# Optimization experiments

Hardware: AMD Instinct MI355X
Metric: run time of the kernel (lower is better)

Reference implementation:

```python
import jax, jax.numpy as jnp
import numpy as np

L, H, NH, PF = 2, 256, 8, 512
D = H // NH
SCALE = float(np.sqrt(D))  # transformerCPI scales by sqrt(hid_dim // n_heads)


def layernorm(x, g, b, eps=1e-5):
    m = x.mean(-1, keepdims=True)
    v = ((x - m) ** 2).mean(-1, keepdims=True)
    return (x - m) / jnp.sqrt(v + eps) * g + b


def mha(q, k, v, wq, bq, wk, bk, wv, bv, wo, bo):
    B, Tq, _ = q.shape
    Tk = k.shape[1]
    Q = (q @ wq + bq).reshape(B, Tq, NH, D).transpose(0, 2, 1, 3)  # [B,h,Tq,d]
    K = (k @ wk + bk).reshape(B, Tk, NH, D).transpose(0, 2, 1, 3)
    V = (v @ wv + bv).reshape(B, Tk, NH, D).transpose(0, 2, 1, 3)
    att = jax.nn.softmax(jnp.einsum('bhqd,bhkd->bhqk', Q, K) / SCALE, axis=-1)
    x = jnp.einsum('bhqk,bhkd->bhqd', att, V).transpose(0, 2, 1, 3).reshape(B, Tq, H)
    return x @ wo + bo, att


def setup_inputs() -> dict:
    key = jax.random.key(0)
    ks = iter(jax.random.split(key, 64))
    B, T, S, A = 16, 512, 1024, 64
    p = lambda shape: jax.random.normal(next(ks), shape, jnp.float32) * 0.02
    inp = {
        'trg': jax.random.normal(next(ks), (B, T, A), jnp.float32),
        'src': jax.random.normal(next(ks), (B, S, H), jnp.float32),
        'ft_w': p((A, H)), 'ft_b': jnp.zeros((H,), jnp.float32),
        'fc1_w': p((H, 256)), 'fc1_b': jnp.zeros((256,), jnp.float32),
        'fc2_w': p((256, 2)), 'fc2_b': jnp.zeros((2,), jnp.float32),
        'ln_g': jnp.ones((L, H), jnp.float32), 'ln_b': jnp.zeros((L, H), jnp.float32),
        'pf_w1': p((L, H, PF)), 'pf_b1': jnp.zeros((L, PF), jnp.float32),
        'pf_w2': p((L, PF, H)), 'pf_b2': jnp.zeros((L, H), jnp.float32),
    }
    for pre in ('sa', 'ea'):
        for nm in ('q', 'k', 'v', 'o'):
            inp[f'{pre}_w{nm}'] = p((L, H, H))
            inp[f'{pre}_b{nm}'] = jnp.zeros((L, H), jnp.float32)
    return inp


def reference(trg, src, ft_w, ft_b, sa_wq, sa_bq, sa_wk, sa_bk, sa_wv, sa_bv, sa_wo, sa_bo,
              ea_wq, ea_bq, ea_wk, ea_bk, ea_wv, ea_bv, ea_wo, ea_bo,
              pf_w1, pf_b1, pf_w2, pf_b2, ln_g, ln_b, fc1_w, fc1_b, fc2_w, fc2_b):
    x = trg @ ft_w + ft_b  # [B,T,H]
    att = None
    for l in range(L):  # small fixed layer count
        sa_out, _ = mha(x, x, x, sa_wq[l], sa_bq[l], sa_wk[l], sa_bk[l],
                        sa_wv[l], sa_bv[l], sa_wo[l], sa_bo[l])
        x = layernorm(x + sa_out, ln_g[l], ln_b[l])
        ea_out, att = mha(x, src, src, ea_wq[l], ea_bq[l], ea_wk[l], ea_bk[l],
                          ea_wv[l], ea_bv[l], ea_wo[l], ea_bo[l])
        x = layernorm(x + ea_out, ln_g[l], ln_b[l])
        ff = jax.nn.relu(x @ pf_w1[l] + pf_b1[l]) @ pf_w2[l] + pf_b2[l]
        x = layernorm(x + ff, ln_g[l], ln_b[l])
    # norm-based softmax pooling (vectorized form of the original double loop)
    w = jax.nn.softmax(jnp.linalg.norm(x, axis=2), axis=1)  # [B,T]
    pooled = jnp.einsum('bt,bth->bh', w, x)                 # [B,H]
    label = jax.nn.relu(pooled @ fc1_w + fc1_b) @ fc2_w + fc2_b  # [B,2]
    return label, pooled, att
```

## Files before the change

### kernel.cpp

```cpp
#include <hip/hip_runtime.h>


typedef __bf16 bfrag __attribute__((ext_vector_type(8)));
typedef float f32x4 __attribute__((ext_vector_type(4)));
typedef unsigned int uint4v __attribute__((ext_vector_type(4)));

__device__ __forceinline__ unsigned short f2bf(float x) {
  unsigned u = __float_as_uint(x);
  u += 0x7fff + ((u >> 16) & 1);
  return (unsigned short)(u >> 16);
}
__device__ __forceinline__ float bf2f(unsigned short h) {
  return __uint_as_float((unsigned)h << 16);
}
__device__ __forceinline__ void split2(float x, unsigned short& hi, unsigned short& lo) {
  hi = f2bf(x);
  lo = f2bf(x - bf2f(hi));
}

__global__ __launch_bounds__(256) void wsplit(
    const float* __restrict__ W, short* __restrict__ Th, short* __restrict__ Tl,
    int K, int N)
{
  __shared__ float t[32][33];
  const int n0 = blockIdx.x * 32, k0 = blockIdx.y * 32;
  const int tx = threadIdx.x & 31, ty = threadIdx.x >> 5;
#pragma unroll
  for (int p = 0; p < 4; p++)
    t[ty + p * 8][tx] = W[(size_t)(k0 + ty + p * 8) * N + n0 + tx];
  __syncthreads();
#pragma unroll
  for (int p = 0; p < 4; p++) {
    float v = t[tx][ty + p * 8];
    unsigned short hi, lo; split2(v, hi, lo);
    size_t o = (size_t)(n0 + ty + p * 8) * K + k0 + tx;
    Th[o] = (short)hi; Tl[o] = (short)lo;
  }
}

__global__ __launch_bounds__(256) void xsplit(
    const float* __restrict__ X, short* __restrict__ Xh, short* __restrict__ Xl,
    int n4)
{
  int i = blockIdx.x * 256 + threadIdx.x;
  if (i < n4) {
    float4 v = ((const float4*)X)[i];
    ushort4 h, l;
    split2(v.x, h.x, l.x); split2(v.y, h.y, l.y);
    split2(v.z, h.z, l.z); split2(v.w, h.w, l.w);
    ((ushort4*)Xh)[i] = h; ((ushort4*)Xl)[i] = l;
  }
}

template <bool RELU, bool SPLIT, bool WRITE_C, bool VT>
__global__ __launch_bounds__(256) void gemm_mfma(
    const short* __restrict__ Ah_g, const short* __restrict__ Al_g,
    const short* __restrict__ Bh_g, const short* __restrict__ Bl_g,
    const float* __restrict__ bias, float* __restrict__ C,
    short* __restrict__ Ch, short* __restrict__ Cl,
    int M, int N, int K, int tksh)
{
  __shared__ short Ah[64 * 40], Al[64 * 40], Bh[64 * 40], Bl[64 * 40];
  const int tid = threadIdx.x;
  const int lane = tid & 63, w = tid >> 6;
  const int wm = w & 1, wn = w >> 1;
  const int m0 = blockIdx.x * 64, n0 = blockIdx.y * 64;
  const int srow = tid >> 2, sc4 = tid & 3;
  const int l15 = lane & 15, l4 = lane >> 4;
  f32x4 acc[2][2] = {};

  for (int k0 = 0; k0 < K; k0 += 32) {
    {
      const size_t ga = (size_t)(m0 + srow) * K + k0 + sc4 * 8;
      const size_t gb = (size_t)(n0 + srow) * K + k0 + sc4 * 8;
      uint4 va_h = *(const uint4*)(Ah_g + ga);
      uint4 va_l = *(const uint4*)(Al_g + ga);
      uint4 vb_h = *(const uint4*)(Bh_g + gb);
      uint4 vb_l = *(const uint4*)(Bl_g + gb);
      const int so = srow * 40 + sc4 * 8;
      *(uint4*)(Ah + so) = va_h;  *(uint4*)(Al + so) = va_l;
      *(uint4*)(Bh + so) = vb_h;  *(uint4*)(Bl + so) = vb_l;
    }
    __syncthreads();
    bfrag af_h[2], af_l[2], bf_h[2], bf_l[2];
#pragma unroll
    for (int mi = 0; mi < 2; mi++) {
      int r = wm * 32 + mi * 16 + l15;
      af_h[mi] = *(const bfrag*)(Ah + r * 40 + l4 * 8);
      af_l[mi] = *(const bfrag*)(Al + r * 40 + l4 * 8);
    }
#pragma unroll
    for (int ni = 0; ni < 2; ni++) {
      int r = wn * 32 + ni * 16 + l15;
      bf_h[ni] = *(const bfrag*)(Bh + r * 40 + l4 * 8);
      bf_l[ni] = *(const bfrag*)(Bl + r * 40 + l4 * 8);
    }
#pragma unroll
    for (int mi = 0; mi < 2; mi++)
#pragma unroll
      for (int ni = 0; ni < 2; ni++) {
        acc[mi][ni] = __builtin_amdgcn_mfma_f32_16x16x32_bf16(af_h[mi], bf_h[ni], acc[mi][ni], 0, 0, 0);
        acc[mi][ni] = __builtin_amdgcn_mfma_f32_16x16x32_bf16(af_h[mi], bf_l[ni], acc[mi][ni], 0, 0, 0);
        acc[mi][ni] = __builtin_amdgcn_mfma_f32_16x16x32_bf16(af_l[mi], bf_h[ni], acc[mi][ni], 0, 0, 0);
      }
    __syncthreads();
  }
#pragma unroll
  for (int mi = 0; mi < 2; mi++)
#pragma unroll
    for (int ni = 0; ni < 2; ni++) {
      const int n = n0 + wn * 32 + ni * 16 + l15;
      const float bv = bias[n];
      if constexpr (VT) {
        const int m = m0 + wm * 32 + mi * 16 + l4 * 4;
        const int bb = m >> tksh, tt = m & ((1 << tksh) - 1);
        const size_t o = ((((size_t)bb * 8 + (n >> 5)) * 32 + (n & 31)) << tksh) + tt;
        unsigned long long wh = 0, wl = 0;
#pragma unroll
        for (int r = 0; r < 4; r++) {
          float v = acc[mi][ni][r] + bv;
          unsigned short hh, ll; split2(v, hh, ll);
          wh |= (unsigned long long)hh << (16 * r);
          wl |= (unsigned long long)ll << (16 * r);
        }
        *(unsigned long long*)(Ch + o) = wh;
        *(unsigned long long*)(Cl + o) = wl;
      } else {
#pragma unroll
        for (int r = 0; r < 4; r++) {
          const int m = m0 + wm * 32 + mi * 16 + l4 * 4 + r;
          float v = acc[mi][ni][r] + bv;
          if (RELU) v = fmaxf(v, 0.f);
          const size_t o = (size_t)m * N + n;
          if constexpr (WRITE_C) C[o] = v;
          if constexpr (SPLIT) {
            unsigned short hh, ll; split2(v, hh, ll);
            Ch[o] = (short)hh; Cl[o] = (short)ll;
          }
        }
      }
    }
}

template <int TK>
__global__ __launch_bounds__(256) void attn_mfma(
    const short* __restrict__ Qh, const short* __restrict__ Ql,
    const short* __restrict__ Kh, const short* __restrict__ Kl,
    const short* __restrict__ Vth, const short* __restrict__ Vtl,
    short* __restrict__ Oh, short* __restrict__ Ol,
    float* __restrict__ att_out)
{
  __shared__ float sc[16 * TK];
  const int b = blockIdx.z, h = blockIdx.y, q0 = blockIdx.x * 16;
  const int tid = threadIdx.x;
  const int lane = tid & 63, w = tid >> 6;
  const int l15 = lane & 15, l4 = lane >> 4;
  const float inv_scale = 0.17677669529663687f;

  const size_t qbase = (((size_t)b * 512 + q0 + l15) * 8 + h) * 32 + l4 * 8;
  bfrag qh = *(const bfrag*)(Qh + qbase);
  bfrag ql = *(const bfrag*)(Ql + qbase);

#pragma unroll 4
  for (int t = 0; t < TK / 64; t++) {
    const int n0c = w * (TK / 4) + t * 16;
    const size_t kbase = (((size_t)b * TK + n0c + l15) * 8 + h) * 32 + l4 * 8;
    bfrag kh = *(const bfrag*)(Kh + kbase);
    bfrag kl = *(const bfrag*)(Kl + kbase);
    f32x4 acc = {};
    acc = __builtin_amdgcn_mfma_f32_16x16x32_bf16(qh, kh, acc, 0, 0, 0);
    acc = __builtin_amdgcn_mfma_f32_16x16x32_bf16(qh, kl, acc, 0, 0, 0);
    acc = __builtin_amdgcn_mfma_f32_16x16x32_bf16(ql, kh, acc, 0, 0, 0);
    const int col = n0c + l15;
#pragma unroll
    for (int r = 0; r < 4; r++) {
      const int row = l4 * 4 + r;
      sc[row * TK + ((((col >> 2) ^ (row & 7)) << 2) | (col & 3))] = acc[r] * inv_scale;
    }
  }
  __syncthreads();

  const int sr = tid >> 4, sj = tid & 15, srsw = sr & 7;
  float mx = -1e30f;
  for (int k = sj; k < TK; k += 16)
    mx = fmaxf(mx, sc[sr * TK + ((((k >> 2) ^ srsw) << 2) | (k & 3))]);
#pragma unroll
  for (int off = 8; off > 0; off >>= 1) mx = fmaxf(mx, __shfl_xor(mx, off, 16));
  float sum = 0.f;
  for (int k = sj; k < TK; k += 16) {
    const int idx = sr * TK + ((((k >> 2) ^ srsw) << 2) | (k & 3));
    float e = __expf(sc[idx] - mx);
    sc[idx] = e;
    sum += e;
  }
#pragma unroll
  for (int off = 8; off > 0; off >>= 1) sum += __shfl_xor(sum, off, 16);
  const float inv = 1.f / sum;
  __syncthreads();

  if (att_out) {
    const size_t orow = (((size_t)(b * 8 + h)) * 512 + q0 + sr) * TK;
    for (int t = 0; t < TK / 64; t++) {
      const int g = sj + 16 * t;
      float4 e4 = *(const float4*)&sc[sr * TK + ((g ^ srsw) << 2)];
      e4.x *= inv; e4.y *= inv; e4.z *= inv; e4.w *= inv;
      *(float4*)&att_out[orow + g * 4] = e4;
    }
  }

  f32x4 oa0 = {}, oa1 = {};
  const float* pr = sc + l15 * TK;
  const int psw = l15 & 7;
  const size_t vb0 = (((size_t)(b * 8 + h)) * 32 + l15) * TK;
  for (int kc = w * (TK / 4); kc < (w + 1) * (TK / 4); kc += 32) {
    const int g0 = (kc >> 2) + l4 * 2;
    float4 p0 = *(const float4*)(pr + ((g0 ^ psw) << 2));
    float4 p1 = *(const float4*)(pr + (((g0 + 1) ^ psw) << 2));
    float f[8] = {p0.x, p0.y, p0.z, p0.w, p1.x, p1.y, p1.z, p1.w};
    uint4v uh, ul;
#pragma unroll
    for (int i = 0; i < 4; i++) {
      unsigned short h0, l0, h1, l1;
      split2(f[2 * i], h0, l0); split2(f[2 * i + 1], h1, l1);
      uh[i] = (unsigned)h0 | ((unsigned)h1 << 16);
      ul[i] = (unsigned)l0 | ((unsigned)l1 << 16);
    }
    bfrag ph = __builtin_bit_cast(bfrag, uh);
    bfrag pl = __builtin_bit_cast(bfrag, ul);
    const size_t vk = vb0 + kc + l4 * 8;
    bfrag v0h = *(const bfrag*)(Vth + vk);
    bfrag v0l = *(const bfrag*)(Vtl + vk);
    bfrag v1h = *(const bfrag*)(Vth + vk + (size_t)16 * TK);
    bfrag v1l = *(const bfrag*)(Vtl + vk + (size_t)16 * TK);
    oa0 = __builtin_amdgcn_mfma_f32_16x16x32_bf16(ph, v0h, oa0, 0, 0, 0);
    oa0 = __builtin_amdgcn_mfma_f32_16x16x32_bf16(ph, v0l, oa0, 0, 0, 0);
    oa0 = __builtin_amdgcn_mfma_f32_16x16x32_bf16(pl, v0h, oa0, 0, 0, 0);
    oa1 = __builtin_amdgcn_mfma_f32_16x16x32_bf16(ph, v1h, oa1, 0, 0, 0);
    oa1 = __builtin_amdgcn_mfma_f32_16x16x32_bf16(ph, v1l, oa1, 0, 0, 0);
    oa1 = __builtin_amdgcn_mfma_f32_16x16x32_bf16(pl, v1h, oa1, 0, 0, 0);
  }
  __syncthreads();
  float* obuf = sc;
#pragma unroll
  for (int r = 0; r < 4; r++) {
    obuf[(w * 16 + l4 * 4 + r) * 32 + l15]      = oa0[r];
    obuf[(w * 16 + l4 * 4 + r) * 32 + 16 + l15] = oa1[r];
  }
  __syncthreads();
  {
    float s0 = 0.f, s1 = 0.f;
#pragma unroll
    for (int ww = 0; ww < 4; ww++) {
      s0 += obuf[(ww * 16 + sr) * 32 + sj];
      s1 += obuf[(ww * 16 + sr) * 32 + 16 + sj];
    }
    s0 *= inv; s1 *= inv;
    unsigned short h0, l0, h1, l1;
    split2(s0, h0, l0); split2(s1, h1, l1);
    const size_t ob = (((size_t)b * 512 + q0 + sr) * 8 + h) * 32 + sj;
    Oh[ob] = (short)h0;      Ol[ob] = (short)l0;
    Oh[ob + 16] = (short)h1; Ol[ob + 16] = (short)l1;
  }
}

__global__ __launch_bounds__(256) void residual_ln(
    float* __restrict__ x, const float* __restrict__ sub,
    const float* __restrict__ g, const float* __restrict__ bi,
    short* __restrict__ xh, short* __restrict__ xl)
{
  __shared__ float red[4];
  const size_t row = blockIdx.x;
  const int tid = threadIdx.x;
  float v = x[row * 256 + tid] + sub[row * 256 + tid];
  float s = v;
  for (int off = 32; off > 0; off >>= 1) s += __shfl_xor(s, off, 64);
  if ((tid & 63) == 0) red[tid >> 6] = s;
  __syncthreads();
  float mean = (red[0] + red[1] + red[2] + red[3]) * (1.f / 256.f);
  float d = v - mean;
  float s2 = d * d;
  for (int off = 32; off > 0; off >>= 1) s2 += __shfl_xor(s2, off, 64);
  __syncthreads();
  if ((tid & 63) == 0) red[tid >> 6] = s2;
  __syncthreads();
  float var = (red[0] + red[1] + red[2] + red[3]) * (1.f / 256.f);
  float y = d * rsqrtf(var + 1e-5f) * g[tid] + bi[tid];
  x[row * 256 + tid] = y;
  unsigned short hh, ll; split2(y, hh, ll);
  xh[row * 256 + tid] = (short)hh;
  xl[row * 256 + tid] = (short)ll;
}

__global__ __launch_bounds__(256) void row_norm(
    const float* __restrict__ x, float* __restrict__ nrm)
{
  __shared__ float red[4];
  const size_t row = blockIdx.x;
  const int tid = threadIdx.x;
  float v = x[row * 256 + tid];
  float s = v * v;
  for (int off = 32; off > 0; off >>= 1) s += __shfl_xor(s, off, 64);
  if ((tid & 63) == 0) red[tid >> 6] = s;
  __syncthreads();
  if (tid == 0) nrm[row] = sqrtf(red[0] + red[1] + red[2] + red[3]);
}

__global__ __launch_bounds__(256) void pool_kernel(
    const float* __restrict__ x, const float* __restrict__ nrm,
    float* __restrict__ pooled, float* __restrict__ pooled_out)
{
  __shared__ float w[512];
  __shared__ float red[4];
  const int b = blockIdx.x, tid = threadIdx.x;
  float n0 = nrm[b * 512 + tid], n1 = nrm[b * 512 + 256 + tid];
  float lm = fmaxf(n0, n1);
  for (int off = 32; off > 0; off >>= 1) lm = fmaxf(lm, __shfl_xor(lm, off, 64));
  if ((tid & 63) == 0) red[tid >> 6] = lm;
  __syncthreads();
  float m = fmaxf(fmaxf(red[0], red[1]), fmaxf(red[2], red[3]));
  float e0 = __expf(n0 - m), e1 = __expf(n1 - m);
  float ls = e0 + e1;
  for (int off = 32; off > 0; off >>= 1) ls += __shfl_xor(ls, off, 64);
  __syncthreads();
  if ((tid & 63) == 0) red[tid >> 6] = ls;
  __syncthreads();
  float inv = 1.f / (red[0] + red[1] + red[2] + red[3]);
  w[tid] = e0 * inv; w[tid + 256] = e1 * inv;
  __syncthreads();
  float acc = 0.f;
  for (int t = 0; t < 512; t++)
    acc += w[t] * x[((size_t)b * 512 + t) * 256 + tid];
  pooled[b * 256 + tid] = acc;
  pooled_out[b * 256 + tid] = acc;
}

__global__ __launch_bounds__(256) void fc_head(
    const float* __restrict__ pooled,
    const float* __restrict__ fc1_w, const float* __restrict__ fc1_b,
    const float* __restrict__ fc2_w, const float* __restrict__ fc2_b,
    float* __restrict__ label_out)
{
  __shared__ float pl[256];
  __shared__ float hid[256];
  const int b = blockIdx.x, tid = threadIdx.x;
  pl[tid] = pooled[b * 256 + tid];
  __syncthreads();
  float acc = fc1_b[tid];
  for (int k = 0; k < 256; k++)
    acc += pl[k] * fc1_w[k * 256 + tid];
  hid[tid] = fmaxf(acc, 0.f);
  __syncthreads();
  if (tid < 2) {
    float s = fc2_b[tid];
    for (int k = 0; k < 256; k++)
      s += hid[k] * fc2_w[k * 2 + tid];
    label_out[b * 2 + tid] = s;
  }
}

extern "C" void kernel_launch(void* const* d_in, const int* in_sizes, int n_in,
                              void* d_out, int out_size, void* d_ws, size_t ws_size,
                              hipStream_t stream)
{
  const float* trg   = (const float*)d_in[0];
  const float* src   = (const float*)d_in[1];
  const float* ft_w  = (const float*)d_in[2];
  const float* ft_b  = (const float*)d_in[3];
  const float* fc1_w = (const float*)d_in[4];
  const float* fc1_b = (const float*)d_in[5];
  const float* fc2_w = (const float*)d_in[6];
  const float* fc2_b = (const float*)d_in[7];
  const float* ln_g  = (const float*)d_in[8];
  const float* ln_b  = (const float*)d_in[9];
  const float* pf_w1 = (const float*)d_in[10];
  const float* pf_b1 = (const float*)d_in[11];
  const float* pf_w2 = (const float*)d_in[12];
  const float* pf_b2 = (const float*)d_in[13];
  const float* aw[2][8];
  for (int p = 0; p < 2; p++)
    for (int i = 0; i < 8; i++) aw[p][i] = (const float*)d_in[14 + p * 8 + i];
  float* outp = (float*)d_out;

  char* wsb = (char*)d_ws;
  const size_t MB = 1u << 20;
  float* x    = (float*)(wsb);
  float* sub  = (float*)(wsb + 8 * MB);
  short* x_hi = (short*)(wsb + 16 * MB);
  short* x_lo = (short*)(wsb + 20 * MB);
  short* qbh  = (short*)(wsb + 24 * MB);
  short* qbl  = (short*)(wsb + 28 * MB);
  short* kbh  = (short*)(wsb + 32 * MB);
  short* kbl  = (short*)(wsb + 40 * MB);
  short* vth  = (short*)(wsb + 48 * MB);
  short* vtl  = (short*)(wsb + 56 * MB);
  short* obh  = (short*)(wsb + 64 * MB);
  short* obl  = (short*)(wsb + 68 * MB);
  short* srch = (short*)(wsb + 72 * MB);
  short* srcl = (short*)(wsb + 80 * MB);
  short* w_hi = (short*)(wsb + 88 * MB);
  short* w_lo = (short*)(wsb + 92 * MB);
  short* ffmh = kbh;
  short* ffml = kbl;
  short* trgh = vth;
  short* trgl = vtl;
  float* nrm  = (float*)qbh;
  float* pld  = (float*)qbh + 8192;

  auto woff = [](int l, int idx) -> size_t {
    size_t base = 16384 + (size_t)l * 786432;
    if (idx < 8)  return base + (size_t)idx * 65536;
    if (idx == 8) return base + 524288;
    return base + 655360;
  };

  wsplit<<<dim3(8, 2), 256, 0, stream>>>(ft_w, w_hi, w_lo, 64, 256);
  for (int l = 0; l < 2; l++) {
    const size_t wo = (size_t)l * 65536;
    for (int i = 0; i < 4; i++)
      wsplit<<<dim3(8, 8), 256, 0, stream>>>(aw[0][2 * i] + wo,
          w_hi + woff(l, i), w_lo + woff(l, i), 256, 256);
    for (int i = 0; i < 4; i++)
      wsplit<<<dim3(8, 8), 256, 0, stream>>>(aw[1][2 * i] + wo,
          w_hi + woff(l, 4 + i), w_lo + woff(l, 4 + i), 256, 256);
    wsplit<<<dim3(16, 8), 256, 0, stream>>>(pf_w1 + (size_t)l * 131072,
        w_hi + woff(l, 8), w_lo + woff(l, 8), 256, 512);
    wsplit<<<dim3(8, 16), 256, 0, stream>>>(pf_w2 + (size_t)l * 131072,
        w_hi + woff(l, 9), w_lo + woff(l, 9), 512, 256);
  }
  xsplit<<<512, 256, 0, stream>>>(trg, trgh, trgl, 131072);
  xsplit<<<4096, 256, 0, stream>>>(src, srch, srcl, 1048576);

  gemm_mfma<false, true, true, false><<<dim3(128, 4), 256, 0, stream>>>(
      trgh, trgl, w_hi, w_lo, ft_b, x, x_hi, x_lo, 8192, 256, 64, 0);

  for (int l = 0; l < 2; l++) {
    const size_t bo = (size_t)l * 256;
    gemm_mfma<false, true, false, false><<<dim3(128, 4), 256, 0, stream>>>(
        x_hi, x_lo, w_hi + woff(l, 0), w_lo + woff(l, 0), aw[0][1] + bo,
        nullptr, qbh, qbl, 8192, 256, 256, 0);
    gemm_mfma<false, true, false, false><<<dim3(128, 4), 256, 0, stream>>>(
        x_hi, x_lo, w_hi + woff(l, 1), w_lo + woff(l, 1), aw[0][3] + bo,
        nullptr, kbh, kbl, 8192, 256, 256, 0);
    gemm_mfma<false, false, false, true><<<dim3(128, 4), 256, 0, stream>>>(
        x_hi, x_lo, w_hi + woff(l, 2), w_lo + woff(l, 2), aw[0][5] + bo,
        nullptr, vth, vtl, 8192, 256, 256, 9);
    attn_mfma<512><<<dim3(32, 8, 16), 256, 0, stream>>>(
        qbh, qbl, kbh, kbl, vth, vtl, obh, obl, (float*)nullptr);
    gemm_mfma<false, false, true, false><<<dim3(128, 4), 256, 0, stream>>>(
        obh, obl, w_hi + woff(l, 3), w_lo + woff(l, 3), aw[0][7] + bo,
        sub, nullptr, nullptr, 8192, 256, 256, 0);
    residual_ln<<<8192, 256, 0, stream>>>(x, sub, ln_g + bo, ln_b + bo, x_hi, x_lo);
    gemm_mfma<false, true, false, false><<<dim3(128, 4), 256, 0, stream>>>(
        x_hi, x_lo, w_hi + woff(l, 4), w_lo + woff(l, 4), aw[1][1] + bo,
        nullptr, qbh, qbl, 8192, 256, 256, 0);
    gemm_mfma<false, true, false, false><<<dim3(256, 4), 256, 0, stream>>>(
        srch, srcl, w_hi + woff(l, 5), w_lo + woff(l, 5), aw[1][3] + bo,
        nullptr, kbh, kbl, 16384, 256, 256, 0);
    gemm_mfma<false, false, false, true><<<dim3(256, 4), 256, 0, stream>>>(
        srch, srcl, w_hi + woff(l, 6), w_lo + woff(l, 6), aw[1][5] + bo,
        nullptr, vth, vtl, 16384, 256, 256, 10);
    {
      float* att = (l == 1) ? (outp + 4128) : (float*)nullptr;
      attn_mfma<1024><<<dim3(32, 8, 16), 256, 0, stream>>>(
          qbh, qbl, kbh, kbl, vth, vtl, obh, obl, att);
    }
    gemm_mfma<false, false, true, false><<<dim3(128, 4), 256, 0, stream>>>(
        obh, obl, w_hi + woff(l, 7), w_lo + woff(l, 7), aw[1][7] + bo,
        sub, nullptr, nullptr, 8192, 256, 256, 0);
    residual_ln<<<8192, 256, 0, stream>>>(x, sub, ln_g + bo, ln_b + bo, x_hi, x_lo);
    gemm_mfma<true, true, false, false><<<dim3(128, 8), 256, 0, stream>>>(
        x_hi, x_lo, w_hi + woff(l, 8), w_lo + woff(l, 8), pf_b1 + (size_t)l * 512,
        nullptr, ffmh, ffml, 8192, 512, 256, 0);
    gemm_mfma<false, false, true, false><<<dim3(128, 4), 256, 0, stream>>>(
        ffmh, ffml, w_hi + woff(l, 9), w_lo + woff(l, 9), pf_b2 + bo,
        sub, nullptr, nullptr, 8192, 256, 512, 0);
    residual_ln<<<8192, 256, 0, stream>>>(x, sub, ln_g + bo, ln_b + bo, x_hi, x_lo);
  }

  row_norm<<<8192, 256, 0, stream>>>(x, nrm);
  pool_kernel<<<16, 256, 0, stream>>>(x, nrm, pld, outp + 32);
  fc_head<<<16, 256, 0, stream>>>(pld, fc1_w, fc1_b, fc2_w, fc2_b, outp);
}
```

Measured before the change: 1.155 ms.

## Fuse QKV/KV projection GEMMs and widen attention blocks with XCD-aware mapping

Merges the separate Q, K and V projection GEMMs into one gemm_qkv launch that picks its bias, destination and transposed-V layout per 64-column segment. This relies on the Q/K/V weight splits being contiguous in the weight buffer. The attention kernel moves from 256 to 512 threads per block and uses a flattened 1D grid. That grid maps blocks so each XCD (chiplet) handles a contiguous range of batch-head pairs for L2 locality. The output-reduction buffer is padded to stride 33 to avoid LDS bank conflicts. Together these cut kernel launches and aim for better parallelism and cache reuse in attention, at the cost of more waves per block and more register and LDS pressure.

```diff
diff --git a/kernel.cpp b/kernel.cpp
--- a/kernel.cpp
+++ b/kernel.cpp
@@ -52,13 +52,51 @@
   }
 }
 
-template <bool RELU, bool SPLIT, bool WRITE_C, bool VT>
+#define GEMM_CORE(Ah_g, Al_g, Bh_g, Bl_g, K)                                   \
+  for (int k0 = 0; k0 < K; k0 += 32) {                                         \
+    {                                                                          \
+      const size_t ga = (size_t)(m0 + srow) * K + k0 + sc4 * 8;                \
+      const size_t gb = (size_t)(n0 + srow) * K + k0 + sc4 * 8;                \
+      uint4 va_h = *(const uint4*)(Ah_g + ga);                                 \
+      uint4 va_l = *(const uint4*)(Al_g + ga);                                 \
+      uint4 vb_h = *(const uint4*)(Bh_g + gb);                                 \
+      uint4 vb_l = *(const uint4*)(Bl_g + gb);                                 \
+      const int so = srow * 40 + sc4 * 8;                                      \
+      *(uint4*)(Ah + so) = va_h;  *(uint4*)(Al + so) = va_l;                   \
+      *(uint4*)(Bh + so) = vb_h;  *(uint4*)(Bl + so) = vb_l;                   \
+    }                                                                          \
+    __syncthreads();                                                           \
+    bfrag af_h[2], af_l[2], bf_h[2], bf_l[2];                                  \
+    _Pragma("unroll")                                                          \
+    for (int mi = 0; mi < 2; mi++) {                                           \
+      int r = wm * 32 + mi * 16 + l15;                                         \
+      af_h[mi] = *(const bfrag*)(Ah + r * 40 + l4 * 8);                        \
+      af_l[mi] = *(const bfrag*)(Al + r * 40 + l4 * 8);                        \
+    }                                                                          \
+    _Pragma("unroll")                                                          \
+    for (int ni = 0; ni < 2; ni++) {                                           \
+      int r = wn * 32 + ni * 16 + l15;                                         \
+      bf_h[ni] = *(const bfrag*)(Bh + r * 40 + l4 * 8);                        \
+      bf_l[ni] = *(const bfrag*)(Bl + r * 40 + l4 * 8);                        \
+    }                                                                          \
+    _Pragma("unroll")                                                          \
+    for (int mi = 0; mi < 2; mi++)                                             \
+      _Pragma("unroll")                                                        \
+      for (int ni = 0; ni < 2; ni++) {                                         \
+        acc[mi][ni] = __builtin_amdgcn_mfma_f32_16x16x32_bf16(af_h[mi], bf_h[ni], acc[mi][ni], 0, 0, 0); \
+        acc[mi][ni] = __builtin_amdgcn_mfma_f32_16x16x32_bf16(af_h[mi], bf_l[ni], acc[mi][ni], 0, 0, 0); \
+        acc[mi][ni] = __builtin_amdgcn_mfma_f32_16x16x32_bf16(af_l[mi], bf_h[ni], acc[mi][ni], 0, 0, 0); \
+      }                                                                        \
+    __syncthreads();                                                           \
+  }
+
+template <bool RELU, bool SPLIT, bool WRITE_C>
 __global__ __launch_bounds__(256) void gemm_mfma(
     const short* __restrict__ Ah_g, const short* __restrict__ Al_g,
     const short* __restrict__ Bh_g, const short* __restrict__ Bl_g,
     const float* __restrict__ bias, float* __restrict__ C,
     short* __restrict__ Ch, short* __restrict__ Cl,
-    int M, int N, int K, int tksh)
+    int M, int N, int K)
 {
   __shared__ short Ah[64 * 40], Al[64 * 40], Bh[64 * 40], Bl[64 * 40];
   const int tid = threadIdx.x;
@@ -68,53 +106,63 @@
   const int srow = tid >> 2, sc4 = tid & 3;
   const int l15 = lane & 15, l4 = lane >> 4;
   f32x4 acc[2][2] = {};
-
-  for (int k0 = 0; k0 < K; k0 += 32) {
-    {
-      const size_t ga = (size_t)(m0 + srow) * K + k0 + sc4 * 8;
-      const size_t gb = (size_t)(n0 + srow) * K + k0 + sc4 * 8;
-      uint4 va_h = *(const uint4*)(Ah_g + ga);
-      uint4 va_l = *(const uint4*)(Al_g + ga);
-      uint4 vb_h = *(const uint4*)(Bh_g + gb);
-      uint4 vb_l = *(const uint4*)(Bl_g + gb);
-      const int so = srow * 40 + sc4 * 8;
-      *(uint4*)(Ah + so) = va_h;  *(uint4*)(Al + so) = va_l;
-      *(uint4*)(Bh + so) = vb_h;  *(uint4*)(Bl + so) = vb_l;
-    }
-    __syncthreads();
-    bfrag af_h[2], af_l[2], bf_h[2], bf_l[2];
-#pragma unroll
-    for (int mi = 0; mi < 2; mi++) {
-      int r = wm * 32 + mi * 16 + l15;
-      af_h[mi] = *(const bfrag*)(Ah + r * 40 + l4 * 8);
-      af_l[mi] = *(const bfrag*)(Al + r * 40 + l4 * 8);
-    }
-#pragma unroll
-    for (int ni = 0; ni < 2; ni++) {
-      int r = wn * 32 + ni * 16 + l15;
-      bf_h[ni] = *(const bfrag*)(Bh + r * 40 + l4 * 8);
-      bf_l[ni] = *(const bfrag*)(Bl + r * 40 + l4 * 8);
-    }
-#pragma unroll
-    for (int mi = 0; mi < 2; mi++)
-#pragma unroll
-      for (int ni = 0; ni < 2; ni++) {
-        acc[mi][ni] = __builtin_amdgcn_mfma_f32_16x16x32_bf16(af_h[mi], bf_h[ni], acc[mi][ni], 0, 0, 0);
-        acc[mi][ni] = __builtin_amdgcn_mfma_f32_16x16x32_bf16(af_h[mi], bf_l[ni], acc[mi][ni], 0, 0, 0);
-        acc[mi][ni] = __builtin_amdgcn_mfma_f32_16x16x32_bf16(af_l[mi], bf_h[ni], acc[mi][ni], 0, 0, 0);
-      }
-    __syncthreads();
-  }
+  GEMM_CORE(Ah_g, Al_g, Bh_g, Bl_g, K)
 #pragma unroll
   for (int mi = 0; mi < 2; mi++)
 #pragma unroll
     for (int ni = 0; ni < 2; ni++) {
       const int n = n0 + wn * 32 + ni * 16 + l15;
       const float bv = bias[n];
-      if constexpr (VT) {
+#pragma unroll
+      for (int r = 0; r < 4; r++) {
+        const int m = m0 + wm * 32 + mi * 16 + l4 * 4 + r;
+        float v = acc[mi][ni][r] + bv;
+        if (RELU) v = fmaxf(v, 0.f);
+        const size_t o = (size_t)m * N + n;
+        if constexpr (WRITE_C) C[o] = v;
+        if constexpr (SPLIT) {
+          unsigned short hh, ll; split2(v, hh, ll);
+          Ch[o] = (short)hh; Cl[o] = (short)ll;
+        }
+      }
+    }
+}
+
+__global__ __launch_bounds__(256) void gemm_qkv(
+    const short* __restrict__ Ah_g, const short* __restrict__ Al_g,
+    const short* __restrict__ Bh_g, const short* __restrict__ Bl_g,
+    const float* __restrict__ b0, const float* __restrict__ b1,
+    const float* __restrict__ b2,
+    short* __restrict__ D0h, short* __restrict__ D0l,
+    short* __restrict__ D1h, short* __restrict__ D1l,
+    short* __restrict__ D2h, short* __restrict__ D2l,
+    int M, int K, int tksh, int nseg)
+{
+  __shared__ short Ah[64 * 40], Al[64 * 40], Bh[64 * 40], Bl[64 * 40];
+  const int tid = threadIdx.x;
+  const int lane = tid & 63, w = tid >> 6;
+  const int wm = w & 1, wn = w >> 1;
+  const int m0 = blockIdx.x * 64, n0 = blockIdx.y * 64;
+  const int srow = tid >> 2, sc4 = tid & 3;
+  const int l15 = lane & 15, l4 = lane >> 4;
+  f32x4 acc[2][2] = {};
+  GEMM_CORE(Ah_g, Al_g, Bh_g, Bl_g, K)
+  const int seg = n0 >> 8;
+  const bool vt = (seg == nseg - 1);
+  const float* bias = (seg == 0) ? b0 : (seg == 1 ? b1 : b2);
+  short* Ch = (seg == 0) ? D0h : (seg == 1 ? D1h : D2h);
+  short* Cl = (seg == 0) ? D0l : (seg == 1 ? D1l : D2l);
+#pragma unroll
+  for (int mi = 0; mi < 2; mi++)
+#pragma unroll
+    for (int ni = 0; ni < 2; ni++) {
+      const int n = n0 + wn * 32 + ni * 16 + l15;
+      const int nl = n & 255;
+      const float bv = bias[nl];
+      if (vt) {
         const int m = m0 + wm * 32 + mi * 16 + l4 * 4;
         const int bb = m >> tksh, tt = m & ((1 << tksh) - 1);
-        const size_t o = ((((size_t)bb * 8 + (n >> 5)) * 32 + (n & 31)) << tksh) + tt;
+        const size_t o = ((((size_t)bb * 8 + (nl >> 5)) * 32 + (nl & 31)) << tksh) + tt;
         unsigned long long wh = 0, wl = 0;
 #pragma unroll
         for (int r = 0; r < 4; r++) {
@@ -130,20 +178,16 @@
         for (int r = 0; r < 4; r++) {
           const int m = m0 + wm * 32 + mi * 16 + l4 * 4 + r;
           float v = acc[mi][ni][r] + bv;
-          if (RELU) v = fmaxf(v, 0.f);
-          const size_t o = (size_t)m * N + n;
-          if constexpr (WRITE_C) C[o] = v;
-          if constexpr (SPLIT) {
-            unsigned short hh, ll; split2(v, hh, ll);
-            Ch[o] = (short)hh; Cl[o] = (short)ll;
-          }
+          unsigned short hh, ll; split2(v, hh, ll);
+          const size_t o = (size_t)m * 256 + nl;
+          Ch[o] = (short)hh; Cl[o] = (short)ll;
         }
       }
     }
 }
 
 template <int TK>
-__global__ __launch_bounds__(256) void attn_mfma(
+__global__ __launch_bounds__(512, 4) void attn_mfma(
     const short* __restrict__ Qh, const short* __restrict__ Ql,
     const short* __restrict__ Kh, const short* __restrict__ Kl,
     const short* __restrict__ Vth, const short* __restrict__ Vtl,
@@ -151,7 +195,11 @@
     float* __restrict__ att_out)
 {
   __shared__ float sc[16 * TK];
-  const int b = blockIdx.z, h = blockIdx.y, q0 = blockIdx.x * 16;
+  const int n = blockIdx.x;
+  const int xcd = n & 7, ii = n >> 3;
+  const int bh = xcd * 16 + (ii >> 5);
+  const int q0 = (ii & 31) * 16;
+  const int b = bh >> 3, h = bh & 7;
   const int tid = threadIdx.x;
   const int lane = tid & 63, w = tid >> 6;
   const int l15 = lane & 15, l4 = lane >> 4;
@@ -161,9 +209,9 @@
   bfrag qh = *(const bfrag*)(Qh + qbase);
   bfrag ql = *(const bfrag*)(Ql + qbase);
 
-#pragma unroll 4
-  for (int t = 0; t < TK / 64; t++) {
-    const int n0c = w * (TK / 4) + t * 16;
+#pragma unroll
+  for (int t = 0; t < TK / 128; t++) {
+    const int n0c = w * (TK / 8) + t * 16;
     const size_t kbase = (((size_t)b * TK + n0c + l15) * 8 + h) * 32 + l4 * 8;
     bfrag kh = *(const bfrag*)(Kh + kbase);
     bfrag kl = *(const bfrag*)(Kl + kbase);
@@ -180,28 +228,29 @@
   }
   __syncthreads();
 
-  const int sr = tid >> 4, sj = tid & 15, srsw = sr & 7;
+  const int sr = tid >> 5, sj = tid & 31, srsw = sr & 7;
   float mx = -1e30f;
-  for (int k = sj; k < TK; k += 16)
+  for (int k = sj; k < TK; k += 32)
     mx = fmaxf(mx, sc[sr * TK + ((((k >> 2) ^ srsw) << 2) | (k & 3))]);
 #pragma unroll
-  for (int off = 8; off > 0; off >>= 1) mx = fmaxf(mx, __shfl_xor(mx, off, 16));
+  for (int off = 16; off > 0; off >>= 1) mx = fmaxf(mx, __shfl_xor(mx, off, 32));
   float sum = 0.f;
-  for (int k = sj; k < TK; k += 16) {
+  for (int k = sj; k < TK; k += 32) {
     const int idx = sr * TK + ((((k >> 2) ^ srsw) << 2) | (k & 3));
     float e = __expf(sc[idx] - mx);
     sc[idx] = e;
     sum += e;
   }
 #pragma unroll
-  for (int off = 8; off > 0; off >>= 1) sum += __shfl_xor(sum, off, 16);
+  for (int off = 16; off > 0; off >>= 1) sum += __shfl_xor(sum, off, 32);
   const float inv = 1.f / sum;
   __syncthreads();
 
   if (att_out) {
     const size_t orow = (((size_t)(b * 8 + h)) * 512 + q0 + sr) * TK;
-    for (int t = 0; t < TK / 64; t++) {
-      const int g = sj + 16 * t;
+#pragma unroll
+    for (int t = 0; t < TK / 128; t++) {
+      const int g = sj + 32 * t;
       float4 e4 = *(const float4*)&sc[sr * TK + ((g ^ srsw) << 2)];
       e4.x *= inv; e4.y *= inv; e4.z *= inv; e4.w *= inv;
       *(float4*)&att_out[orow + g * 4] = e4;
@@ -212,7 +261,8 @@
   const float* pr = sc + l15 * TK;
   const int psw = l15 & 7;
   const size_t vb0 = (((size_t)(b * 8 + h)) * 32 + l15) * TK;
-  for (int kc = w * (TK / 4); kc < (w + 1) * (TK / 4); kc += 32) {
+#pragma unroll
+  for (int kc = w * (TK / 8); kc < (w + 1) * (TK / 8); kc += 32) {
     const int g0 = (kc >> 2) + l4 * 2;
     float4 p0 = *(const float4*)(pr + ((g0 ^ psw) << 2));
     float4 p1 = *(const float4*)(pr + (((g0 + 1) ^ psw) << 2));
@@ -243,23 +293,20 @@
   float* obuf = sc;
 #pragma unroll
   for (int r = 0; r < 4; r++) {
-    obuf[(w * 16 + l4 * 4 + r) * 32 + l15]      = oa0[r];
-    obuf[(w * 16 + l4 * 4 + r) * 32 + 16 + l15] = oa1[r];
+    obuf[(w * 16 + l4 * 4 + r) * 33 + l15]      = oa0[r];
+    obuf[(w * 16 + l4 * 4 + r) * 33 + 16 + l15] = oa1[r];
   }
   __syncthreads();
   {
-    float s0 = 0.f, s1 = 0.f;
-#pragma unroll
-    for (int ww = 0; ww < 4; ww++) {
-      s0 += obuf[(ww * 16 + sr) * 32 + sj];
-      s1 += obuf[(ww * 16 + sr) * 32 + 16 + sj];
-    }
-    s0 *= inv; s1 *= inv;
-    unsigned short h0, l0, h1, l1;
-    split2(s0, h0, l0); split2(s1, h1, l1);
+    float s0 = 0.f;
+#pragma unroll
+    for (int ww = 0; ww < 8; ww++)
+      s0 += obuf[(ww * 16 + sr) * 33 + sj];
+    s0 *= inv;
+    unsigned short h0, l0;
+    split2(s0, h0, l0);
     const size_t ob = (((size_t)b * 512 + q0 + sr) * 8 + h) * 32 + sj;
-    Oh[ob] = (short)h0;      Ol[ob] = (short)l0;
-    Oh[ob + 16] = (short)h1; Ol[ob + 16] = (short)l1;
+    Oh[ob] = (short)h0;  Ol[ob] = (short)l0;
   }
 }
 
@@ -430,50 +477,43 @@
   xsplit<<<512, 256, 0, stream>>>(trg, trgh, trgl, 131072);
   xsplit<<<4096, 256, 0, stream>>>(src, srch, srcl, 1048576);
 
-  gemm_mfma<false, true, true, false><<<dim3(128, 4), 256, 0, stream>>>(
-      trgh, trgl, w_hi, w_lo, ft_b, x, x_hi, x_lo, 8192, 256, 64, 0);
+  gemm_mfma<false, true, true><<<dim3(128, 4), 256, 0, stream>>>(
+      trgh, trgl, w_hi, w_lo, ft_b, x, x_hi, x_lo, 8192, 256, 64);
 
   for (int l = 0; l < 2; l++) {
     const size_t bo = (size_t)l * 256;
-    gemm_mfma<false, true, false, false><<<dim3(128, 4), 256, 0, stream>>>(
-        x_hi, x_lo, w_hi + woff(l, 0), w_lo + woff(l, 0), aw[0][1] + bo,
-        nullptr, qbh, qbl, 8192, 256, 256, 0);
-    gemm_mfma<false, true, false, false><<<dim3(128, 4), 256, 0, stream>>>(
-        x_hi, x_lo, w_hi + woff(l, 1), w_lo + woff(l, 1), aw[0][3] + bo,
-        nullptr, kbh, kbl, 8192, 256, 256, 0);
-    gemm_mfma<false, false, false, true><<<dim3(128, 4), 256, 0, stream>>>(
-        x_hi, x_lo, w_hi + woff(l, 2), w_lo + woff(l, 2), aw[0][5] + bo,
-        nullptr, vth, vtl, 8192, 256, 256, 9);
-    attn_mfma<512><<<dim3(32, 8, 16), 256, 0, stream>>>(
+    gemm_qkv<<<dim3(128, 12), 256, 0, stream>>>(
+        x_hi, x_lo, w_hi + woff(l, 0), w_lo + woff(l, 0),
+        aw[0][1] + bo, aw[0][3] + bo, aw[0][5] + bo,
+        qbh, qbl, kbh, kbl, vth, vtl, 8192, 256, 9, 3);
+    attn_mfma<512><<<4096, 512, 0, stream>>>(
         qbh, qbl, kbh, kbl, vth, vtl, obh, obl, (float*)nullptr);
-    gemm_mfma<false, false, true, false><<<dim3(128, 4), 256, 0, stream>>>(
+    gemm_mfma<false, false, true><<<dim3(128, 4), 256, 0, stream>>>(
         obh, obl, w_hi + woff(l, 3), w_lo + woff(l, 3), aw[0][7] + bo,
-        sub, nullptr, nullptr, 8192, 256, 256, 0);
+        sub, nullptr, nullptr, 8192, 256, 256);
     residual_ln<<<8192, 256, 0, stream>>>(x, sub, ln_g + bo, ln_b + bo, x_hi, x_lo);
-    gemm_mfma<false, true, false, false><<<dim3(128, 4), 256, 0, stream>>>(
+    gemm_mfma<false, true, false><<<dim3(128, 4), 256, 0, stream>>>(
         x_hi, x_lo, w_hi + woff(l, 4), w_lo + woff(l, 4), aw[1][1] + bo,
-        nullptr, qbh, qbl, 8192, 256, 256, 0);
-    gemm_mfma<false, true, false, false><<<dim3(256, 4), 256, 0, stream>>>(
-        srch, srcl, w_hi + woff(l, 5), w_lo + woff(l, 5), aw[1][3] + bo,
-        nullptr, kbh, kbl, 16384, 256, 256, 0);
-    gemm_mfma<false, false, false, true><<<dim3(256, 4), 256, 0, stream>>>(
-        srch, srcl, w_hi + woff(l, 6), w_lo + woff(l, 6), aw[1][5] + bo,
-        nullptr, vth, vtl, 16384, 256, 256, 10);
+        nullptr, qbh, qbl, 8192, 256, 256);
+    gemm_qkv<<<dim3(256, 8), 256, 0, stream>>>(
+        srch, srcl, w_hi + woff(l, 5), w_lo + woff(l, 5),
+        aw[1][3] + bo, aw[1][5] + bo, nullptr,
+        kbh, kbl, vth, vtl, nullptr, nullptr, 16384, 256, 10, 2);
     {
       float* att = (l == 1) ? (outp + 4128) : (float*)nullptr;
-      attn_mfma<1024><<<dim3(32, 8, 16), 256, 0, stream>>>(
+      attn_mfma<1024><<<4096, 512, 0, stream>>>(
           qbh, qbl, kbh, kbl, vth, vtl, obh, obl, att);
     }
-    gemm_mfma<false, false, true, false><<<dim3(128, 4), 256, 0, stream>>>(
+    gemm_mfma<false, false, true><<<dim3(128, 4), 256, 0, stream>>>(
         obh, obl, w_hi + woff(l, 7), w_lo + woff(l, 7), aw[1][7] + bo,
-        sub, nullptr, nullptr, 8192, 256, 256, 0);
+        sub, nullptr, nullptr, 8192, 256, 256);
     residual_ln<<<8192, 256, 0, stream>>>(x, sub, ln_g + bo, ln_b + bo, x_hi, x_lo);
-    gemm_mfma<true, true, false, false><<<dim3(128, 8), 256, 0, stream>>>(
+    gemm_mfma<true, true, false><<<dim3(128, 8), 256, 0, stream>>>(
         x_hi, x_lo, w_hi + woff(l, 8), w_lo + woff(l, 8), pf_b1 + (size_t)l * 512,
-        nullptr, ffmh, ffml, 8192, 512, 256, 0);
-    gemm_mfma<false, false, true, false><<<dim3(128, 4), 256, 0, stream>>>(
+        nullptr, ffmh, ffml, 8192, 512, 256);
+    gemm_mfma<false, false, true><<<dim3(128, 4), 256, 0, stream>>>(
         ffmh, ffml, w_hi + woff(l, 9), w_lo + woff(l, 9), pf_b2 + bo,
-        sub, nullptr, nullptr, 8192, 256, 512, 0);
+        sub, nullptr, nullptr, 8192, 256, 512);
     residual_ln<<<8192, 256, 0, stream>>>(x, sub, ln_g + bo, ln_b + bo, x_hi, x_lo);
   }
 
```

New measurement: 1.085 ms. 1.06x faster.
